# Kernel optimization log

Hardware: AMD Instinct MI355X
Metric: run time of the kernel (lower is better)

Reference implementation:

```python
import jax, jax.numpy as jnp
import numpy as np
import math

B, T, D = 4, 8192, 512
E, K, F = 8, 2, 2048
CAP_FACTOR = 1.25


def setup_inputs() -> dict:
    key = jax.random.key(0)
    ks = jax.random.split(key, 4)
    return {
        "x": jax.random.normal(ks[0], (B, T, D), jnp.float32),
        "gate_w": jax.random.normal(ks[1], (E, D), jnp.float32) * 0.01,  # std=0.01 init
        "w1": jax.random.normal(ks[2], (E, D, F), jnp.float32) * (1.0 / np.sqrt(D)),
        "b1": jnp.zeros((E, F), jnp.float32),
        "w2": jax.random.normal(ks[3], (E, F, D), jnp.float32) * (1.0 / np.sqrt(F)),
        "b2": jnp.zeros((E, D), jnp.float32),
    }


def reference(x, gate_w, w1, b1, w2, b2):
    Bx, Tx, Dx = x.shape
    N = Bx * Tx
    C = math.ceil(CAP_FACTOR * N / E)  # per-expert capacity
    xf = x.reshape(N, Dx)

    # --- Router (eval mode: no noise) ---
    probs = jax.nn.softmax(xf @ gate_w.T, axis=-1)            # (N, E)
    topk_vals, topk_idx = jax.lax.top_k(probs, K)             # (N, K)
    topk_vals = topk_vals / topk_vals.sum(-1, keepdims=True)

    # --- Capacity-based dispatch: token-major, k-minor assignment order,
    #     matching the original serial double loop exactly. ---
    flat_e = topk_idx.reshape(N * K)                          # (NK,)
    onehot = jax.nn.one_hot(flat_e, E, dtype=jnp.int32)       # (NK, E)
    # slot within expert = number of earlier assignments to same expert
    pos = jnp.cumsum(onehot, axis=0)[jnp.arange(N * K), flat_e] - 1
    keep = pos < C                                            # tokens over capacity are dropped
    pos_safe = jnp.where(keep, pos, C)                        # route drops to pad slot C
    token_ids = jnp.repeat(jnp.arange(N), K)

    # --- Gather tokens into (E, C, D) expert buffers (slot C is trash) ---
    buf = jnp.zeros((E, C + 1, Dx), x.dtype).at[flat_e, pos_safe].set(xf[token_ids])
    expert_in = buf[:, :C]                                    # (E, C, D)

    # --- Per-expert FFN (exact GELU, dropout=0 in eval) ---
    h = jax.nn.gelu(jnp.einsum('ecd,edf->ecf', expert_in, w1) + b1[:, None, :],
                    approximate=False)                        # (E, C, F)
    expert_out = jnp.einsum('ecf,efd->ecd', h, w2) + b2[:, None, :]  # (E, C, D)

    # --- Weighted combine back to tokens ---
    gathered = expert_out[flat_e, jnp.minimum(pos_safe, C - 1)]      # (NK, D)
    w = (topk_vals.reshape(N * K) * keep).astype(x.dtype)            # zero for dropped
    out = (gathered * w[:, None]).reshape(N, K, Dx).sum(axis=1)      # (N, D)
    return out.reshape(Bx, Tx, Dx)
```

## Files before the change

### kernel.cpp

```cpp
#include <hip/hip_runtime.h>
#include <math.h>

#define Bx 4
#define Tt 8192
#define Nn (Bx * Tt)
#define Dd 512
#define Ee 8
#define Kk 2
#define Ff 2048
#define Cc 5120
#define NK (Nn * Kk)

typedef unsigned short ushort_t;
typedef __attribute__((ext_vector_type(8))) short bf16x8;
typedef __attribute__((ext_vector_type(4))) float f32x4;

__device__ __forceinline__ float gelu_exact(float v) {
    return 0.5f * v * (1.0f + erff(v * 0.70710678118654752440f));
}

__device__ __forceinline__ ushort_t f2bf(float f) {
    union { float f; unsigned u; } v; v.f = f;
    unsigned r = v.u + 0x7fffu + ((v.u >> 16) & 1u);
    return (ushort_t)(r >> 16);
}

__device__ __forceinline__ void gload_lds16(const ushort_t* g, short* l) {
    __builtin_amdgcn_global_load_lds(
        (const __attribute__((address_space(1))) unsigned int*)g,
        (__attribute__((address_space(3))) unsigned int*)l, 16, 0, 0);
}

__global__ __launch_bounds__(256) void moe_gate_kernel(
    const float* __restrict__ x, const float* __restrict__ gate_w,
    int* __restrict__ flat_e, float* __restrict__ wArr) {
    __shared__ float gw[Ee * Dd];
    int tid = threadIdx.x;
    for (int i = tid; i < 1024; i += 256)
        ((float4*)gw)[i] = ((const float4*)gate_w)[i];
    __syncthreads();

    int wave = tid >> 6, lane = tid & 63;
    int token = blockIdx.x * 4 + wave;

    const float4* xr = (const float4*)(x + (size_t)token * Dd);
    float4 xa = xr[lane];
    float4 xb = xr[lane + 64];

    float acc[Ee];
#pragma unroll
    for (int e = 0; e < Ee; e++) {
        const float4* g = (const float4*)(gw + e * Dd);
        float4 ga = g[lane], gb = g[lane + 64];
        acc[e] = xa.x * ga.x + xa.y * ga.y + xa.z * ga.z + xa.w * ga.w +
                 xb.x * gb.x + xb.y * gb.y + xb.z * gb.z + xb.w * gb.w;
    }
#pragma unroll
    for (int off = 32; off >= 1; off >>= 1) {
#pragma unroll
        for (int e = 0; e < Ee; e++) acc[e] += __shfl_xor(acc[e], off, 64);
    }

    if (lane == 0) {
        float m = acc[0];
#pragma unroll
        for (int e = 1; e < Ee; e++) m = fmaxf(m, acc[e]);
        float p[Ee], s = 0.f;
#pragma unroll
        for (int e = 0; e < Ee; e++) { p[e] = expf(acc[e] - m); s += p[e]; }
        int i0 = 0;
#pragma unroll
        for (int e = 1; e < Ee; e++) if (p[e] > p[i0]) i0 = e;
        int i1 = (i0 == 0) ? 1 : 0;
#pragma unroll
        for (int e = 0; e < Ee; e++) if (e != i0 && p[e] > p[i1]) i1 = e;
        float v0 = p[i0] / s, v1 = p[i1] / s;
        float inv = 1.f / (v0 + v1);
        flat_e[token * 2 + 0] = i0;
        flat_e[token * 2 + 1] = i1;
        wArr[token * 2 + 0] = v0 * inv;
        wArr[token * 2 + 1] = v1 * inv;
    }
}

__global__ __launch_bounds__(256) void moe_hist_kernel(
    const int* __restrict__ flat_e, int* __restrict__ blockCounts) {
    __shared__ int cnt[Ee];
    int tid = threadIdx.x;
    if (tid < Ee) cnt[tid] = 0;
    __syncthreads();
    int e = flat_e[blockIdx.x * 256 + tid];
    atomicAdd(&cnt[e], 1);
    __syncthreads();
    if (tid < Ee) blockCounts[blockIdx.x * Ee + tid] = cnt[tid];
}

__global__ void moe_scan_kernel(const int* __restrict__ blockCounts,
                                int* __restrict__ blockOffsets,
                                int* __restrict__ counts) {
    int e = threadIdx.x;
    if (e >= Ee) return;
    int run = 0;
    for (int b = 0; b < 256; b++) {
        blockOffsets[b * Ee + e] = run;
        run += blockCounts[b * Ee + e];
    }
    counts[e] = min(run, Cc);
}

__global__ __launch_bounds__(256) void moe_scatter_kernel(
    const int* __restrict__ flat_e, const float* __restrict__ wArr,
    const int* __restrict__ blockOffsets,
    int* __restrict__ srcOf, float* __restrict__ wSlot) {
    __shared__ int waveCnt[4][Ee];
    int tid = threadIdx.x;
    int i = blockIdx.x * 256 + tid;
    int e = flat_e[i];
    int wv = tid >> 6, lane = tid & 63;
    unsigned long long ltmask = (1ull << lane) - 1ull;
    int myrank = 0;
#pragma unroll
    for (int ee = 0; ee < Ee; ee++) {
        unsigned long long m = __ballot(e == ee);
        if (e == ee) myrank = __popcll(m & ltmask);
        if (lane == 0) waveCnt[wv][ee] = __popcll(m);
    }
    __syncthreads();
    int base = blockOffsets[blockIdx.x * Ee + e];
    for (int w = 0; w < wv; w++) base += waveCnt[w][e];
    int pos = base + myrank;
    if (pos < Cc) {
        srcOf[e * Cc + pos] = i >> 1;
        wSlot[e * Cc + pos] = wArr[i];
    }
}

__global__ __launch_bounds__(256) void moe_transpose_kernel(
    const float* __restrict__ in, ushort_t* __restrict__ out, int R, int Cn) {
    __shared__ float t[32][33];
    int ez = blockIdx.z;
    const float* ine = in + (size_t)ez * R * Cn;
    ushort_t* oute = out + (size_t)ez * R * Cn;
    int tx = threadIdx.x & 31, ty = threadIdx.x >> 5;
    int r0 = blockIdx.y * 32, c0 = blockIdx.x * 32;
#pragma unroll
    for (int j = 0; j < 4; j++)
        t[ty + j * 8][tx] = ine[(size_t)(r0 + ty + j * 8) * Cn + c0 + tx];
    __syncthreads();
#pragma unroll
    for (int j = 0; j < 4; j++)
        oute[(size_t)(c0 + ty + j * 8) * R + r0 + tx] = f2bf(t[tx][ty + j * 8]);
}

__global__ __launch_bounds__(256) void moe_gather_kernel(
    const float* __restrict__ x, const int* __restrict__ srcOf,
    const int* __restrict__ counts, int chunk0, ushort_t* __restrict__ xg) {
    int tid = threadIdx.x, wave = tid >> 6, lane = tid & 63;
    int sl = blockIdx.x * 4 + wave;
    int le = sl / Cc, c = sl - le * Cc;
    int e = chunk0 + le;
    int cnt = counts[e];
    ushort_t* dst = xg + (size_t)sl * Dd + lane * 8;
    uint4 o;
    if (c < cnt) {
        int src = srcOf[e * Cc + c];
        const float4* xr = (const float4*)(x + (size_t)src * Dd + lane * 8);
        float4 v0 = xr[0], v1 = xr[1];
        o.x = (unsigned)f2bf(v0.x) | ((unsigned)f2bf(v0.y) << 16);
        o.y = (unsigned)f2bf(v0.z) | ((unsigned)f2bf(v0.w) << 16);
        o.z = (unsigned)f2bf(v1.x) | ((unsigned)f2bf(v1.y) << 16);
        o.w = (unsigned)f2bf(v1.z) | ((unsigned)f2bf(v1.w) << 16);
    } else {
        o = make_uint4(0, 0, 0, 0);
    }
    *(uint4*)dst = o;
}


#define GSTAGE(gA, gB, Al, Bl, buf, t, wbase)                                  \
    do {                                                                       \
        int _k = (t) * 32;                                                     \
        gload_lds16((gA) + _k,      &(Al)[(buf) * 4096 + (wbase)]);            \
        gload_lds16((gA) + _k + 16, &(Al)[(buf) * 4096 + 2048 + (wbase)]);     \
        gload_lds16((gB) + _k,      &(Bl)[(buf) * 4096 + (wbase)]);            \
        gload_lds16((gB) + _k + 16, &(Bl)[(buf) * 4096 + 2048 + (wbase)]);     \
    } while (0)

__global__ __launch_bounds__(256) void moe_mfma_gemm1(
    const ushort_t* __restrict__ xg, const ushort_t* __restrict__ w1t,
    const float* __restrict__ b1, int chunk0, ushort_t* __restrict__ hbuf) {
    int le = blockIdx.z, e = chunk0 + le;
    const ushort_t* A = xg + (size_t)le * Cc * Dd;
    const ushort_t* Bt = w1t + (size_t)e * Ff * Dd;
    const float* bias = b1 + (size_t)e * Ff;
    ushort_t* h = hbuf + (size_t)le * Cc * Ff;

    __shared__ short Al[2 * 4096];
    __shared__ short Bl[2 * 4096];

    int tid = threadIdx.x;
    int lane = tid & 63, wave = tid >> 6;
    int wr = wave >> 1, wc = wave & 1;
    int m0 = blockIdx.y * 128;
    int n0 = blockIdx.x * 128;
    int kslot = lane >> 4, lr = lane & 15;
    int aoff = (kslot * 128 + wr * 64 + lr) * 8;
    int boff = (kslot * 128 + wc * 64 + lr) * 8;
    int wbase = (tid & 192) * 8;
    int row = tid & 127, ks0 = tid >> 7;

    const ushort_t* gA = A + (size_t)(m0 + row) * Dd + ks0 * 8;
    const ushort_t* gB = Bt + (size_t)(n0 + row) * Dd + ks0 * 8;

    f32x4 acc[4][4] = {};
    const int NT = Dd / 32;

    GSTAGE(gA, gB, Al, Bl, 0, 0, wbase);
    for (int t = 0; t < NT; ++t) {
        int cur = t & 1;
        if (t + 1 < NT) {
            GSTAGE(gA, gB, Al, Bl, cur ^ 1, t + 1, wbase);
            asm volatile("s_waitcnt vmcnt(4)" ::: "memory");
        } else {
            asm volatile("s_waitcnt vmcnt(0)" ::: "memory");
        }
        __builtin_amdgcn_s_barrier();
        asm volatile("" ::: "memory");
        bf16x8 a[4], b[4];
        int ab = cur * 4096 + aoff, bb = cur * 4096 + boff;
#pragma unroll
        for (int m = 0; m < 4; ++m) a[m] = *(const bf16x8*)&Al[ab + m * 128];
#pragma unroll
        for (int n = 0; n < 4; ++n) b[n] = *(const bf16x8*)&Bl[bb + n * 128];
#pragma unroll
        for (int m = 0; m < 4; ++m)
#pragma unroll
            for (int n = 0; n < 4; ++n)
                acc[m][n] = __builtin_amdgcn_mfma_f32_16x16x32_bf16(
                    a[m], b[n], acc[m][n], 0, 0, 0);
        asm volatile("" ::: "memory");
        __builtin_amdgcn_s_barrier();
    }

    float bv[4];
#pragma unroll
    for (int n = 0; n < 4; ++n) bv[n] = bias[n0 + wc * 64 + n * 16 + lr];
#pragma unroll
    for (int m = 0; m < 4; ++m) {
#pragma unroll
        for (int r = 0; r < 4; ++r) {
            int orow = m0 + wr * 64 + m * 16 + kslot * 4 + r;
            size_t base = (size_t)orow * Ff + n0 + wc * 64 + lr;
#pragma unroll
            for (int n = 0; n < 4; ++n)
                h[base + n * 16] = f2bf(gelu_exact(acc[m][n][r] + bv[n]));
        }
    }
}

__global__ __launch_bounds__(256) void moe_mfma_gemm2(
    const ushort_t* __restrict__ hbuf, const ushort_t* __restrict__ w2t,
    const float* __restrict__ b2, const int* __restrict__ srcOf,
    const float* __restrict__ wSlot, const int* __restrict__ counts,
    int chunk0, float* __restrict__ out) {
    int z = blockIdx.z;
    int le = z >> 1, ksp = z & 1;
    int e = chunk0 + le;
    const int KH = Ff / 2;
    const ushort_t* A = hbuf + (size_t)le * Cc * Ff + (size_t)ksp * KH;
    const ushort_t* Bt = w2t + (size_t)e * Dd * Ff + (size_t)ksp * KH;
    const float* bias = b2 + (size_t)e * Dd;
    const int* srcE = srcOf + (size_t)e * Cc;
    const float* wE = wSlot + (size_t)e * Cc;
    int count = counts[e];

    __shared__ short Al[2 * 4096];
    __shared__ short Bl[2 * 4096];

    int tid = threadIdx.x;
    int lane = tid & 63, wave = tid >> 6;
    int wr = wave >> 1, wc = wave & 1;
    int m0 = blockIdx.y * 128;
    int n0 = blockIdx.x * 128;
    int kslot = lane >> 4, lr = lane & 15;
    int aoff = (kslot * 128 + wr * 64 + lr) * 8;
    int boff = (kslot * 128 + wc * 64 + lr) * 8;
    int wbase = (tid & 192) * 8;
    int row = tid & 127, ks0 = tid >> 7;

    const ushort_t* gA = A + (size_t)(m0 + row) * Ff + ks0 * 8;
    const ushort_t* gB = Bt + (size_t)(n0 + row) * Ff + ks0 * 8;

    f32x4 acc[4][4] = {};
    const int NT = KH / 32;

    GSTAGE(gA, gB, Al, Bl, 0, 0, wbase);
    for (int t = 0; t < NT; ++t) {
        int cur = t & 1;
        if (t + 1 < NT) {
            GSTAGE(gA, gB, Al, Bl, cur ^ 1, t + 1, wbase);
            asm volatile("s_waitcnt vmcnt(4)" ::: "memory");
        } else {
            asm volatile("s_waitcnt vmcnt(0)" ::: "memory");
        }
        __builtin_amdgcn_s_barrier();
        asm volatile("" ::: "memory");
        bf16x8 a[4], b[4];
        int ab = cur * 4096 + aoff, bb = cur * 4096 + boff;
#pragma unroll
        for (int m = 0; m < 4; ++m) a[m] = *(const bf16x8*)&Al[ab + m * 128];
#pragma unroll
        for (int n = 0; n < 4; ++n) b[n] = *(const bf16x8*)&Bl[bb + n * 128];
#pragma unroll
        for (int m = 0; m < 4; ++m)
#pragma unroll
            for (int n = 0; n < 4; ++n)
                acc[m][n] = __builtin_amdgcn_mfma_f32_16x16x32_bf16(
                    a[m], b[n], acc[m][n], 0, 0, 0);
        asm volatile("" ::: "memory");
        __builtin_amdgcn_s_barrier();
    }

    float bv[4];
#pragma unroll
    for (int n = 0; n < 4; ++n)
        bv[n] = (ksp == 0) ? bias[n0 + wc * 64 + n * 16 + lr] : 0.f;
#pragma unroll
    for (int m = 0; m < 4; ++m) {
#pragma unroll
        for (int r = 0; r < 4; ++r) {
            int orow = m0 + wr * 64 + m * 16 + kslot * 4 + r;
            if (orow < count) {
                int token = srcE[orow];
                float wgt = wE[orow];
                float* op = out + (size_t)token * Dd + n0 + wc * 64 + lr;
#pragma unroll
                for (int n = 0; n < 4; ++n)
                    atomicAdd(&op[n * 16], wgt * (acc[m][n][r] + bv[n]));
            }
        }
    }
}

extern "C" void kernel_launch(void* const* d_in, const int* in_sizes, int n_in,
                              void* d_out, int out_size, void* d_ws, size_t ws_size,
                              hipStream_t stream) {
    const float* x      = (const float*)d_in[0];
    const float* gate_w = (const float*)d_in[1];
    const float* w1     = (const float*)d_in[2];
    const float* b1     = (const float*)d_in[3];
    const float* w2     = (const float*)d_in[4];
    const float* b2     = (const float*)d_in[5];
    float* out = (float*)d_out;

    char* p = (char*)d_ws;
    int*      flat_e       = (int*)p;       p += (size_t)NK * 4;
    float*    wArr         = (float*)p;     p += (size_t)NK * 4;
    int*      blockCounts  = (int*)p;       p += 256 * Ee * 4;
    int*      blockOffsets = (int*)p;       p += 256 * Ee * 4;
    int*      counts       = (int*)p;       p += 64 * 4;
    int*      srcOf        = (int*)p;       p += (size_t)Ee * Cc * 4;
    float*    wSlot        = (float*)p;     p += (size_t)Ee * Cc * 4;
    p = (char*)(((size_t)p + 255) & ~(size_t)255);
    ushort_t* w1t          = (ushort_t*)p;  p += (size_t)Ee * Dd * Ff * 2;
    ushort_t* w2t          = (ushort_t*)p;  p += (size_t)Ee * Ff * Dd * 2;
    size_t fixedEnd = (size_t)(p - (char*)d_ws);
    size_t avail = (ws_size > fixedEnd) ? ws_size - fixedEnd : 0;

    size_t perE = (size_t)Cc * Dd * 2 + (size_t)Cc * Ff * 2;
    int P = Ee;
    while (P > 1 && (size_t)P * perE > avail) P >>= 1;
    ushort_t* xg = (ushort_t*)((char*)d_ws + fixedEnd);
    ushort_t* hbuf = xg + (size_t)P * Cc * Dd;

    moe_gate_kernel<<<Nn / 4, 256, 0, stream>>>(x, gate_w, flat_e, wArr);
    moe_hist_kernel<<<NK / 256, 256, 0, stream>>>(flat_e, blockCounts);
    moe_scan_kernel<<<1, 64, 0, stream>>>(blockCounts, blockOffsets, counts);
    moe_scatter_kernel<<<NK / 256, 256, 0, stream>>>(flat_e, wArr, blockOffsets,
                                                     srcOf, wSlot);
    moe_transpose_kernel<<<dim3(Ff / 32, Dd / 32, Ee), 256, 0, stream>>>(
        w1, w1t, Dd, Ff);
    moe_transpose_kernel<<<dim3(Dd / 32, Ff / 32, Ee), 256, 0, stream>>>(
        w2, w2t, Ff, Dd);
    hipMemsetAsync(d_out, 0, (size_t)Nn * Dd * sizeof(float), stream);

    for (int c0 = 0; c0 < Ee; c0 += P) {
        moe_gather_kernel<<<P * Cc / 4, 256, 0, stream>>>(x, srcOf, counts, c0, xg);
        moe_mfma_gemm1<<<dim3(Ff / 128, Cc / 128, P), 256, 0, stream>>>(
            xg, w1t, b1, c0, hbuf);
        moe_mfma_gemm2<<<dim3(Dd / 128, Cc / 128, P * 2), 256, 0, stream>>>(
            hbuf, w2t, b2, srcOf, wSlot, counts, c0, out);
    }
}
```

Baseline: 708.3 us.

## Swizzle GEMM block order across XCDs and drop split-K in second GEMM

Adds a block-id swizzle that remaps the linear workgroup id so consecutive tiles land on the same XCD (stride-8 interleave), aiming for better L2 reuse of weight and activation tiles in both expert GEMMs. It also removes the two-way split-K from the second GEMM, so each block covers the full F dimension and half as many blocks issue atomic adds to the output. The trade is fewer blocks in GEMM2 (lower occupancy/parallelism) and longer per-block loops. The swizzle assumes the workgroup count divides evenly by 8.

```diff
diff --git a/kernel.cpp b/kernel.cpp
--- a/kernel.cpp
+++ b/kernel.cpp
@@ -29,6 +29,15 @@
     __builtin_amdgcn_global_load_lds(
         (const __attribute__((address_space(1))) unsigned int*)g,
         (__attribute__((address_space(3))) unsigned int*)l, 16, 0, 0);
+}
+
+__device__ __forceinline__ void swz_decode(int gx, int gy, int& x, int& y, int& z) {
+    int nwg = gridDim.x * gridDim.y * gridDim.z;
+    int orig = blockIdx.x + gridDim.x * (blockIdx.y + gridDim.y * blockIdx.z);
+    int cpx = nwg >> 3;
+    int id = (orig & 7) * cpx + (orig >> 3);
+    x = id % gx; id /= gx;
+    y = id % gy; z = id / gy;
 }
 
 __global__ __launch_bounds__(256) void moe_gate_kernel(
@@ -189,7 +198,9 @@
 __global__ __launch_bounds__(256) void moe_mfma_gemm1(
     const ushort_t* __restrict__ xg, const ushort_t* __restrict__ w1t,
     const float* __restrict__ b1, int chunk0, ushort_t* __restrict__ hbuf) {
-    int le = blockIdx.z, e = chunk0 + le;
+    int bx, by, le;
+    swz_decode(Ff / 128, Cc / 128, bx, by, le);
+    int e = chunk0 + le;
     const ushort_t* A = xg + (size_t)le * Cc * Dd;
     const ushort_t* Bt = w1t + (size_t)e * Ff * Dd;
     const float* bias = b1 + (size_t)e * Ff;
@@ -201,8 +212,8 @@
     int tid = threadIdx.x;
     int lane = tid & 63, wave = tid >> 6;
     int wr = wave >> 1, wc = wave & 1;
-    int m0 = blockIdx.y * 128;
-    int n0 = blockIdx.x * 128;
+    int m0 = by * 128;
+    int n0 = bx * 128;
     int kslot = lane >> 4, lr = lane & 15;
     int aoff = (kslot * 128 + wr * 64 + lr) * 8;
     int boff = (kslot * 128 + wc * 64 + lr) * 8;
@@ -263,12 +274,11 @@
     const float* __restrict__ b2, const int* __restrict__ srcOf,
     const float* __restrict__ wSlot, const int* __restrict__ counts,
     int chunk0, float* __restrict__ out) {
-    int z = blockIdx.z;
-    int le = z >> 1, ksp = z & 1;
+    int bx, by, le;
+    swz_decode(Dd / 128, Cc / 128, bx, by, le);
     int e = chunk0 + le;
-    const int KH = Ff / 2;
-    const ushort_t* A = hbuf + (size_t)le * Cc * Ff + (size_t)ksp * KH;
-    const ushort_t* Bt = w2t + (size_t)e * Dd * Ff + (size_t)ksp * KH;
+    const ushort_t* A = hbuf + (size_t)le * Cc * Ff;
+    const ushort_t* Bt = w2t + (size_t)e * Dd * Ff;
     const float* bias = b2 + (size_t)e * Dd;
     const int* srcE = srcOf + (size_t)e * Cc;
     const float* wE = wSlot + (size_t)e * Cc;
@@ -280,8 +290,8 @@
     int tid = threadIdx.x;
     int lane = tid & 63, wave = tid >> 6;
     int wr = wave >> 1, wc = wave & 1;
-    int m0 = blockIdx.y * 128;
-    int n0 = blockIdx.x * 128;
+    int m0 = by * 128;
+    int n0 = bx * 128;
     int kslot = lane >> 4, lr = lane & 15;
     int aoff = (kslot * 128 + wr * 64 + lr) * 8;
     int boff = (kslot * 128 + wc * 64 + lr) * 8;
@@ -292,7 +302,7 @@
     const ushort_t* gB = Bt + (size_t)(n0 + row) * Ff + ks0 * 8;
 
     f32x4 acc[4][4] = {};
-    const int NT = KH / 32;
+    const int NT = Ff / 32;
 
     GSTAGE(gA, gB, Al, Bl, 0, 0, wbase);
     for (int t = 0; t < NT; ++t) {
@@ -323,8 +333,7 @@
 
     float bv[4];
 #pragma unroll
-    for (int n = 0; n < 4; ++n)
-        bv[n] = (ksp == 0) ? bias[n0 + wc * 64 + n * 16 + lr] : 0.f;
+    for (int n = 0; n < 4; ++n) bv[n] = bias[n0 + wc * 64 + n * 16 + lr];
 #pragma unroll
     for (int m = 0; m < 4; ++m) {
 #pragma unroll
@@ -388,7 +397,7 @@
         moe_gather_kernel<<<P * Cc / 4, 256, 0, stream>>>(x, srcOf, counts, c0, xg);
         moe_mfma_gemm1<<<dim3(Ff / 128, Cc / 128, P), 256, 0, stream>>>(
             xg, w1t, b1, c0, hbuf);
-        moe_mfma_gemm2<<<dim3(Dd / 128, Cc / 128, P * 2), 256, 0, stream>>>(
+        moe_mfma_gemm2<<<dim3(Dd / 128, Cc / 128, P), 256, 0, stream>>>(
             hbuf, w2t, b2, srcOf, wSlot, counts, c0, out);
     }
 }
```

New measurement: 653.3 us. 1.08x faster.
